# Optimization experiments

Measured on AMD Instinct MI355X. Metric: run time of the kernel, lower is better.

The kernel has to match this reference:

```python
import jax, jax.numpy as jnp
import numpy as np

EMBD_SIZE = 128
NUM_HEADS = 8
HEAD_SIZE = 16

def setup_inputs() -> dict:
    key = jax.random.key(0)
    ks = jax.random.split(key, 6)
    B, S = 8, 2048
    x = jax.random.normal(ks[0], (B, S, EMBD_SIZE), dtype=jnp.float32)
    # per-head Linear weights, torch layout [out, in] stacked over heads -> [H, hs, E]
    sc = 1.0 / np.sqrt(EMBD_SIZE)
    Wk = jax.random.normal(ks[1], (NUM_HEADS, HEAD_SIZE, EMBD_SIZE), dtype=jnp.float32) * sc
    Wq = jax.random.normal(ks[2], (NUM_HEADS, HEAD_SIZE, EMBD_SIZE), dtype=jnp.float32) * sc
    Wv = jax.random.normal(ks[3], (NUM_HEADS, HEAD_SIZE, EMBD_SIZE), dtype=jnp.float32) * sc
    Wp = jax.random.normal(ks[4], (EMBD_SIZE, NUM_HEADS * HEAD_SIZE), dtype=jnp.float32) * sc
    bp = jax.random.normal(ks[5], (EMBD_SIZE,), dtype=jnp.float32) * 0.01
    return {"x": x, "Wk": Wk, "Wq": Wq, "Wv": Wv, "Wp": Wp, "bp": bp}

def reference(x, Wk, Wq, Wv, Wp, bp):
    # x: [B,S,E]; W{k,q,v}: [H,hs,E]; Wp: [E,H*hs]
    B, S, E = x.shape
    H, hs, _ = Wk.shape
    q = jnp.einsum('bse,hde->bhsd', x, Wq)
    k = jnp.einsum('bse,hde->bhsd', x, Wk)
    v = jnp.einsum('bse,hde->bhsd', x, Wv)
    # NOTE: original code MULTIPLIES by sqrt(head_size) (k.shape[-1]**0.5)
    scores = jnp.einsum('bhsd,bhtd->bhst', q, k) * (hs ** 0.5)
    wei = jax.nn.softmax(scores, axis=-1)  # dropout is identity in eval mode
    out = jnp.einsum('bhst,bhtd->bhsd', wei, v)
    # concat heads along last dim: [B,S,H*hs]
    out = out.transpose(0, 2, 1, 3).reshape(B, S, H * hs)
    return out @ Wp.T + bp
```

## Files before the change

### kernel.cpp

```cpp
#include <hip/hip_runtime.h>
#include <hip/hip_bf16.h>

constexpr int Bb  = 8;
constexpr int Ss  = 2048;
constexpr int Ee  = 128;
constexpr int Hh  = 8;
constexpr int HSs = 16;
constexpr int QKVSZ = Bb * Hh * Ss * HSs;

typedef _Float16 f16;
typedef __attribute__((ext_vector_type(8)))  _Float16 f16x8;
typedef __attribute__((ext_vector_type(16))) float f32x16;

constexpr float QSCALE = 5.770780163555854f;

__device__ __forceinline__ unsigned pack_rtz(float lo, float hi) {
    union { __fp16 __attribute__((ext_vector_type(2))) h; unsigned u; } c;
    c.h = __builtin_amdgcn_cvt_pkrtz(lo, hi);
    return c.u;
}
__device__ __forceinline__ unsigned pack_rne(float lo, float hi) {
    union { __attribute__((ext_vector_type(2))) _Float16 h; unsigned u; } c;
    c.h[0] = (f16)lo; c.h[1] = (f16)hi;
    return c.u;
}

__global__ __launch_bounds__(256) void prep_w(
    const float* __restrict__ Wq, const float* __restrict__ Wk,
    const float* __restrict__ Wv, const float* __restrict__ Wp,
    f16* __restrict__ wh)
{
    int i = (blockIdx.x * 256 + threadIdx.x) * 4;
    const float* src = (i < 16384) ? (Wq + i)
                     : (i < 32768) ? (Wk + i - 16384)
                     : (i < 49152) ? (Wv + i - 32768) : (Wp + i - 49152);
    float4 v = *(const float4*)src;
    union { f16 h[4]; uint2 u; } c;
    c.h[0] = (f16)v.x; c.h[1] = (f16)v.y; c.h[2] = (f16)v.z; c.h[3] = (f16)v.w;
    *(uint2*)(wh + i) = c.u;
}

__global__ __launch_bounds__(256) void qkv_kernel(
    const float* __restrict__ x, const f16* __restrict__ wh,
    f16* __restrict__ qo, f16* __restrict__ ko, f16* __restrict__ vo)
{
    constexpr int LDW = 136;
    __shared__ __align__(16) f16 Xs[32 * LDW];

    const int mat = blockIdx.y;
    const int rowbase = blockIdx.x * 32;

    for (int idx = threadIdx.x; idx < 32 * 32; idx += 256) {
        const int r = idx >> 5, cp = idx & 31;
        float4 v = *(const float4*)(x + (size_t)(rowbase + r) * Ee + cp * 4);
        union { f16 h[4]; uint2 u; } c;
        c.h[0] = (f16)v.x; c.h[1] = (f16)v.y; c.h[2] = (f16)v.z; c.h[3] = (f16)v.w;
        *(uint2*)&Xs[r * LDW + cp * 4] = c.u;
    }
    __syncthreads();

    const int wv_ = threadIdx.x >> 6, lane = threadIdx.x & 63;
    const int h = lane >> 5, n31 = lane & 31;

    f16x8 A[8];
#pragma unroll
    for (int t = 0; t < 8; ++t)
        A[t] = *(const f16x8*)&Xs[n31 * LDW + 16 * t + 8 * h];

    const int c = wv_ * 32 + n31;
    const f16* wr = wh + mat * 16384 + (size_t)c * Ee + 8 * h;
    f32x16 acc = {};
#pragma unroll
    for (int t = 0; t < 8; ++t)
        acc = __builtin_amdgcn_mfma_f32_32x32x16_f16(A[t], *(const f16x8*)(wr + 16 * t), acc, 0, 0, 0);

    const int b = rowbase >> 11;
    const int s0 = rowbase & 2047;
    const int head = c >> 4, d = c & 15;
    const int bh = b * Hh + head;

    if (mat < 2) {
        f16* dst = (mat == 0) ? qo : ko;
        const float scale = (mat == 1) ? QSCALE : 1.f;
#pragma unroll
        for (int r = 0; r < 16; ++r) {
            const int s = s0 + (r & 3) + 8 * (r >> 2) + 4 * h;
            dst[((size_t)bh * Ss + s) * HSs + d] = (f16)(acc[r] * scale);
        }
    } else {
        const int it = s0 >> 6, g0 = (s0 >> 4) & 3;
        f16* vb = vo + (size_t)bh * 65536 + it * 2048;
#pragma unroll
        for (int rq = 0; rq < 4; ++rq) {
            union { f16 hv[4]; uint2 u; } pk4;
#pragma unroll
            for (int i = 0; i < 4; ++i) pk4.hv[i] = (f16)acc[4 * rq + i];
            *(uint2*)(vb + (g0 + (rq >> 1)) * 512 + (d + 32 * (rq & 1)) * 8 + 4 * h) = pk4.u;
        }
        for (int i = threadIdx.x; i < 512; i += 256) {
            const int gp = i >> 8, hd = (i >> 5) & 7, cc = i & 31;
            const int lanep = (cc < 16) ? 16 + cc : 32 + cc;
            const unsigned one2 = 0x3C003C00u;
            uint4 val = ((cc & 15) == 0) ? (uint4){one2, one2, one2, one2}
                                         : (uint4){0, 0, 0, 0};
            *(uint4*)(vo + (size_t)(b * Hh + hd) * 65536 + it * 2048
                      + (g0 + gp) * 512 + lanep * 8) = val;
        }
    }
}

__device__ __forceinline__ void cb_exchange(const unsigned* pw, int h,
                                            f16x8& Blo, f16x8& Bhi) {
    unsigned exa = (unsigned)__shfl_xor((int)(h ? pw[0] : pw[2]), 32, 64);
    unsigned exb = (unsigned)__shfl_xor((int)(h ? pw[1] : pw[3]), 32, 64);
    unsigned exc = (unsigned)__shfl_xor((int)(h ? pw[4] : pw[6]), 32, 64);
    unsigned exd = (unsigned)__shfl_xor((int)(h ? pw[5] : pw[7]), 32, 64);
    union { unsigned u[4]; f16x8 v; } B1, B2;
    if (h == 0) {
        B1.u[0] = pw[0]; B1.u[1] = pw[1]; B1.u[2] = exa; B1.u[3] = exb;
        B2.u[0] = pw[4]; B2.u[1] = pw[5]; B2.u[2] = exc; B2.u[3] = exd;
    } else {
        B1.u[0] = exa; B1.u[1] = exb; B1.u[2] = pw[2]; B1.u[3] = pw[3];
        B2.u[0] = exc; B2.u[1] = exd; B2.u[2] = pw[6]; B2.u[3] = pw[7];
    }
    Blo = B1.v; Bhi = B2.v;
}

__global__ __launch_bounds__(64, 4) void attn_kernel(
    const f16* __restrict__ qg, const f16* __restrict__ kg,
    const f16* __restrict__ vg, f16* __restrict__ og)
{
    const int blk  = blockIdx.x;
    const int bh   = (blk & 7) * 8 + (blk >> 9);
    const int qblk = (blk >> 3) & 63;
    const int lane = threadIdx.x;
    const int h    = lane >> 5;
    const int q31  = lane & 31;
    const int qbase = qblk * 32;

    const f16x8 qf = *(const f16x8*)(qg + ((size_t)bh * Ss + qbase + q31) * HSs + 8 * h);

    const f16* pk = kg + (size_t)bh * Ss * HSs + q31 * 16 + 8 * h;
    const f16* pv = vg + (size_t)bh * 65536 + lane * 8;

    f16x8 ka0 = *(const f16x8*)pk;
    f16x8 ka1 = *(const f16x8*)(pk + 512);
    f16x8 va0 = *(const f16x8*)(pv);
    f16x8 va1 = *(const f16x8*)(pv + 512);
    f16x8 va2 = *(const f16x8*)(pv + 1024);
    f16x8 va3 = *(const f16x8*)(pv + 1536);

    f32x16 acc = {};
    const f32x16 z16 = {};
    float m = -1e30f;

    for (int it = 0; it < Ss / 64; ++it) {
        f16x8 nk0, nk1, nv0, nv1, nv2, nv3;
        if (it < Ss / 64 - 1) {
            pk += 1024; pv += 2048;
            nk0 = *(const f16x8*)pk;
            nk1 = *(const f16x8*)(pk + 512);
            nv0 = *(const f16x8*)(pv);
            nv1 = *(const f16x8*)(pv + 512);
            nv2 = *(const f16x8*)(pv + 1024);
            nv3 = *(const f16x8*)(pv + 1536);
        }

        f32x16 st0 = __builtin_amdgcn_mfma_f32_32x32x16_f16(ka0, qf, z16, 0, 0, 0);
        f32x16 st1 = __builtin_amdgcn_mfma_f32_32x32x16_f16(ka1, qf, z16, 0, 0, 0);

        float mx = st0[0];
#pragma unroll
        for (int t = 1; t < 16; ++t) mx = fmaxf(mx, st0[t]);
#pragma unroll
        for (int t = 0; t < 16; ++t) mx = fmaxf(mx, st1[t]);
        mx = fmaxf(mx, __shfl_xor(mx, 32, 64));
        const float mnew = fmaxf(m, mx);
        const float corr = __builtin_amdgcn_exp2f(m - mnew);
#pragma unroll
        for (int r = 0; r < 9; ++r) acc[r] *= corr;
        m = mnew;

#pragma unroll
        for (int t = 0; t < 16; ++t) st0[t] = __builtin_amdgcn_exp2f(st0[t] - mnew);
#pragma unroll
        for (int t = 0; t < 16; ++t) st1[t] = __builtin_amdgcn_exp2f(st1[t] - mnew);
        unsigned pw0[8], pw1[8];
#pragma unroll
        for (int r = 0; r < 8; ++r) pw0[r] = pack_rtz(st0[2 * r], st0[2 * r + 1]);
#pragma unroll
        for (int r = 0; r < 8; ++r) pw1[r] = pack_rtz(st1[2 * r], st1[2 * r + 1]);
        f16x8 B1, B2, B3, B4;
        cb_exchange(pw0, h, B1, B2);
        cb_exchange(pw1, h, B3, B4);

        acc = __builtin_amdgcn_mfma_f32_32x32x16_f16(va0, B1, acc, 0, 0, 0);
        acc = __builtin_amdgcn_mfma_f32_32x32x16_f16(va1, B2, acc, 0, 0, 0);
        acc = __builtin_amdgcn_mfma_f32_32x32x16_f16(va2, B3, acc, 0, 0, 0);
        acc = __builtin_amdgcn_mfma_f32_32x32x16_f16(va3, B4, acc, 0, 0, 0);

        ka0 = nk0; ka1 = nk1;
        va0 = nv0; va1 = nv1; va2 = nv2; va3 = nv3;
    }

    const float l = acc[8] + __shfl_xor(acc[8], 32, 64);
    const float inv = 1.f / l;
    const int b = bh >> 3, head = bh & 7;
    f16* op = og + ((size_t)b * Ss + qbase + q31) * Ee + head * HSs;
    uint2 lo = { pack_rne(acc[0] * inv, acc[1] * inv), pack_rne(acc[2] * inv, acc[3] * inv) };
    uint2 hi = { pack_rne(acc[4] * inv, acc[5] * inv), pack_rne(acc[6] * inv, acc[7] * inv) };
    *(uint2*)(op + 4 * h)     = lo;
    *(uint2*)(op + 8 + 4 * h) = hi;
}

__global__ __launch_bounds__(256) void proj_kernel(
    const f16* __restrict__ oh, const f16* __restrict__ wph,
    const float* __restrict__ bp, float* __restrict__ out)
{
    constexpr int LDW = 136;
    __shared__ __align__(16) f16 Os[32 * LDW];
    const int rowbase = blockIdx.x * 32;

    for (int idx = threadIdx.x; idx < 512; idx += 256) {
        const int r = idx >> 4, cp = idx & 15;
        *(f16x8*)&Os[r * LDW + cp * 8] =
            *(const f16x8*)(oh + (size_t)(rowbase + r) * Ee + cp * 8);
    }
    __syncthreads();

    const int wv_ = threadIdx.x >> 6, lane = threadIdx.x & 63;
    const int h = lane >> 5, n31 = lane & 31;

    f16x8 A[8];
#pragma unroll
    for (int t = 0; t < 8; ++t)
        A[t] = *(const f16x8*)&Os[n31 * LDW + 16 * t + 8 * h];

    const int e = wv_ * 32 + n31;
    const f16* wr = wph + (size_t)e * Ee + 8 * h;
    f32x16 acc = {};
#pragma unroll
    for (int t = 0; t < 8; ++t)
        acc = __builtin_amdgcn_mfma_f32_32x32x16_f16(A[t], *(const f16x8*)(wr + 16 * t), acc, 0, 0, 0);

    const float bias = bp[e];
#pragma unroll
    for (int r = 0; r < 16; ++r) {
        const int R = rowbase + (r & 3) + 8 * (r >> 2) + 4 * h;
        out[(size_t)R * Ee + e] = acc[r] + bias;
    }
}

extern "C" void kernel_launch(void* const* d_in, const int* in_sizes, int n_in,
                              void* d_out, int out_size, void* d_ws, size_t ws_size,
                              hipStream_t stream)
{
    const float* x  = (const float*)d_in[0];
    const float* Wk = (const float*)d_in[1];
    const float* Wq = (const float*)d_in[2];
    const float* Wv = (const float*)d_in[3];
    const float* Wp = (const float*)d_in[4];
    const float* bp = (const float*)d_in[5];
    float* out = (float*)d_out;

    f16* ws = (f16*)d_ws;
    f16* qh = ws;
    f16* kh = ws + (size_t)QKVSZ;
    f16* vh = ws + (size_t)2 * QKVSZ;
    f16* oh = ws + (size_t)4 * QKVSZ;
    f16* wh = ws + (size_t)5 * QKVSZ;

    prep_w<<<64, 256, 0, stream>>>(Wq, Wk, Wv, Wp, wh);
    qkv_kernel<<<dim3(Bb * Ss / 32, 3), 256, 0, stream>>>(x, wh, qh, kh, vh);
    attn_kernel<<<Bb * Hh * (Ss / 32), 64, 0, stream>>>(qh, kh, vh, oh);
    proj_kernel<<<Bb * Ss / 32, 256, 0, stream>>>(oh, wh + 49152, bp, out);
}
```

Before: 137.6 us.

## Split attention KV range across two waves and fuse QKV into one pass

The attention kernel now runs two waves per block, each covering half the key/value sequence. Their partial softmax states are merged through shared memory, which doubles parallelism per query tile and halves the serial loop length. The QKV kernel computes all three projections in one block, reusing the loaded x tile instead of reloading it for each matrix. V is staged through shared memory so it can be written as coalesced 16-byte stores, and the constant ones/zeros padding of the V layout moves into the prep kernel. The cost is an extra shared-memory combine step and more register pressure in the attention blocks.

Result: slower. 321.0 us (+133.2%).

```diff
diff --git a/kernel.cpp b/kernel.cpp
--- a/kernel.cpp
+++ b/kernel.cpp
@@ -25,19 +25,30 @@
     return c.u;
 }
 
-__global__ __launch_bounds__(256) void prep_w(
+__global__ __launch_bounds__(256) void prep_kernel(
     const float* __restrict__ Wq, const float* __restrict__ Wk,
     const float* __restrict__ Wv, const float* __restrict__ Wp,
-    f16* __restrict__ wh)
-{
-    int i = (blockIdx.x * 256 + threadIdx.x) * 4;
-    const float* src = (i < 16384) ? (Wq + i)
-                     : (i < 32768) ? (Wk + i - 16384)
-                     : (i < 49152) ? (Wv + i - 32768) : (Wp + i - 49152);
-    float4 v = *(const float4*)src;
-    union { f16 h[4]; uint2 u; } c;
-    c.h[0] = (f16)v.x; c.h[1] = (f16)v.y; c.h[2] = (f16)v.z; c.h[3] = (f16)v.w;
-    *(uint2*)(wh + i) = c.u;
+    f16* __restrict__ wh, f16* __restrict__ vo)
+{
+    const int idx = blockIdx.x * 256 + threadIdx.x;
+    if (idx < 16384) {
+        const int i = idx * 4;
+        const float* src = (i < 16384) ? (Wq + i)
+                         : (i < 32768) ? (Wk + i - 16384)
+                         : (i < 49152) ? (Wv + i - 32768) : (Wp + i - 49152);
+        float4 v = *(const float4*)src;
+        union { f16 h[4]; uint2 u; } c;
+        c.h[0] = (f16)v.x; c.h[1] = (f16)v.y; c.h[2] = (f16)v.z; c.h[3] = (f16)v.w;
+        *(uint2*)(wh + i) = c.u;
+    } else {
+        const int p = idx - 16384;
+        const int lane32 = p & 31, g = (p >> 5) & 3, it = (p >> 7) & 31, bh = p >> 12;
+        const int lanep = 16 + (lane32 & 15) + (lane32 >> 4) * 32;
+        const unsigned one2 = 0x3C003C00u;
+        uint4 val = ((lane32 & 15) == 0) ? (uint4){one2, one2, one2, one2}
+                                         : (uint4){0, 0, 0, 0};
+        *(uint4*)(vo + (size_t)bh * 65536 + it * 2048 + g * 512 + lanep * 8) = val;
+    }
 }
 
 __global__ __launch_bounds__(256) void qkv_kernel(
@@ -47,7 +58,6 @@
     constexpr int LDW = 136;
     __shared__ __align__(16) f16 Xs[32 * LDW];
 
-    const int mat = blockIdx.y;
     const int rowbase = blockIdx.x * 32;
 
     for (int idx = threadIdx.x; idx < 32 * 32; idx += 256) {
@@ -66,20 +76,34 @@
 #pragma unroll
     for (int t = 0; t < 8; ++t)
         A[t] = *(const f16x8*)&Xs[n31 * LDW + 16 * t + 8 * h];
+    __syncthreads();
 
     const int c = wv_ * 32 + n31;
-    const f16* wr = wh + mat * 16384 + (size_t)c * Ee + 8 * h;
-    f32x16 acc = {};
-#pragma unroll
-    for (int t = 0; t < 8; ++t)
-        acc = __builtin_amdgcn_mfma_f32_32x32x16_f16(A[t], *(const f16x8*)(wr + 16 * t), acc, 0, 0, 0);
-
     const int b = rowbase >> 11;
     const int s0 = rowbase & 2047;
     const int head = c >> 4, d = c & 15;
     const int bh = b * Hh + head;
 
-    if (mat < 2) {
+    {
+        const f16* wr = wh + 2 * 16384 + (size_t)c * Ee + 8 * h;
+        f32x16 acc = {};
+#pragma unroll
+        for (int t = 0; t < 8; ++t)
+            acc = __builtin_amdgcn_mfma_f32_32x32x16_f16(A[t], *(const f16x8*)(wr + 16 * t), acc, 0, 0, 0);
+#pragma unroll
+        for (int r = 0; r < 16; ++r) {
+            const int row = (r & 3) + 8 * (r >> 2) + 4 * h;
+            Xs[row * LDW + c] = (f16)acc[r];
+        }
+    }
+
+#pragma unroll
+    for (int mat = 0; mat < 2; ++mat) {
+        const f16* wr = wh + mat * 16384 + (size_t)c * Ee + 8 * h;
+        f32x16 acc = {};
+#pragma unroll
+        for (int t = 0; t < 8; ++t)
+            acc = __builtin_amdgcn_mfma_f32_32x32x16_f16(A[t], *(const f16x8*)(wr + 16 * t), acc, 0, 0, 0);
         f16* dst = (mat == 0) ? qo : ko;
         const float scale = (mat == 1) ? QSCALE : 1.f;
 #pragma unroll
@@ -87,25 +111,18 @@
             const int s = s0 + (r & 3) + 8 * (r >> 2) + 4 * h;
             dst[((size_t)bh * Ss + s) * HSs + d] = (f16)(acc[r] * scale);
         }
-    } else {
-        const int it = s0 >> 6, g0 = (s0 >> 4) & 3;
-        f16* vb = vo + (size_t)bh * 65536 + it * 2048;
-#pragma unroll
-        for (int rq = 0; rq < 4; ++rq) {
-            union { f16 hv[4]; uint2 u; } pk4;
-#pragma unroll
-            for (int i = 0; i < 4; ++i) pk4.hv[i] = (f16)acc[4 * rq + i];
-            *(uint2*)(vb + (g0 + (rq >> 1)) * 512 + (d + 32 * (rq & 1)) * 8 + 4 * h) = pk4.u;
-        }
-        for (int i = threadIdx.x; i < 512; i += 256) {
-            const int gp = i >> 8, hd = (i >> 5) & 7, cc = i & 31;
-            const int lanep = (cc < 16) ? 16 + cc : 32 + cc;
-            const unsigned one2 = 0x3C003C00u;
-            uint4 val = ((cc & 15) == 0) ? (uint4){one2, one2, one2, one2}
-                                         : (uint4){0, 0, 0, 0};
-            *(uint4*)(vo + (size_t)(b * Hh + hd) * 65536 + it * 2048
-                      + (g0 + gp) * 512 + lanep * 8) = val;
-        }
+    }
+    __syncthreads();
+
+    const int it = s0 >> 6, g0 = (s0 >> 4) & 3;
+    for (int p = threadIdx.x; p < 512; p += 256) {
+        const int gl = p >> 8, hd = (p >> 5) & 7, dd = (p >> 1) & 15, eh = p & 1;
+        union { f16 hv[8]; uint4 u; } pkt;
+#pragma unroll
+        for (int j = 0; j < 8; ++j)
+            pkt.hv[j] = Xs[(gl * 16 + eh * 8 + j) * LDW + hd * 16 + dd];
+        *(uint4*)(vo + (size_t)(b * Hh + hd) * 65536 + it * 2048
+                  + (g0 + gl) * 512 + (dd + 32 * eh) * 8) = pkt.u;
     }
 }
 
@@ -126,22 +143,25 @@
     Blo = B1.v; Bhi = B2.v;
 }
 
-__global__ __launch_bounds__(64, 4) void attn_kernel(
+__global__ __launch_bounds__(128, 6) void attn_kernel(
     const f16* __restrict__ qg, const f16* __restrict__ kg,
     const f16* __restrict__ vg, f16* __restrict__ og)
 {
+    __shared__ float cmb[32 * 20];
+
     const int blk  = blockIdx.x;
     const int bh   = (blk & 7) * 8 + (blk >> 9);
     const int qblk = (blk >> 3) & 63;
-    const int lane = threadIdx.x;
+    const int wv_  = threadIdx.x >> 6;
+    const int lane = threadIdx.x & 63;
     const int h    = lane >> 5;
     const int q31  = lane & 31;
     const int qbase = qblk * 32;
 
     const f16x8 qf = *(const f16x8*)(qg + ((size_t)bh * Ss + qbase + q31) * HSs + 8 * h);
 
-    const f16* pk = kg + (size_t)bh * Ss * HSs + q31 * 16 + 8 * h;
-    const f16* pv = vg + (size_t)bh * 65536 + lane * 8;
+    const f16* pk = kg + (size_t)bh * Ss * HSs + wv_ * 1024 * HSs + q31 * 16 + 8 * h;
+    const f16* pv = vg + (size_t)bh * 65536 + wv_ * 32768 + lane * 8;
 
     f16x8 ka0 = *(const f16x8*)pk;
     f16x8 ka1 = *(const f16x8*)(pk + 512);
@@ -154,9 +174,9 @@
     const f32x16 z16 = {};
     float m = -1e30f;
 
-    for (int it = 0; it < Ss / 64; ++it) {
+    for (int it = 0; it < 16; ++it) {
         f16x8 nk0, nk1, nv0, nv1, nv2, nv3;
-        if (it < Ss / 64 - 1) {
+        if (it < 15) {
             pk += 1024; pv += 2048;
             nk0 = *(const f16x8*)pk;
             nk1 = *(const f16x8*)(pk + 512);
@@ -169,11 +189,13 @@
         f32x16 st0 = __builtin_amdgcn_mfma_f32_32x32x16_f16(ka0, qf, z16, 0, 0, 0);
         f32x16 st1 = __builtin_amdgcn_mfma_f32_32x32x16_f16(ka1, qf, z16, 0, 0, 0);
 
-        float mx = st0[0];
-#pragma unroll
-        for (int t = 1; t < 16; ++t) mx = fmaxf(mx, st0[t]);
-#pragma unroll
-        for (int t = 0; t < 16; ++t) mx = fmaxf(mx, st1[t]);
+        float t0[8];
+#pragma unroll
+        for (int t = 0; t < 8; ++t)
+            t0[t] = fmaxf(fmaxf(st0[t], st0[t + 8]), fmaxf(st1[t], st1[t + 8]));
+#pragma unroll
+        for (int t = 0; t < 4; ++t) t0[t] = fmaxf(t0[t], t0[t + 4]);
+        float mx = fmaxf(fmaxf(t0[0], t0[1]), fmaxf(t0[2], t0[3]));
         mx = fmaxf(mx, __shfl_xor(mx, 32, 64));
         const float mnew = fmaxf(m, mx);
         const float corr = __builtin_amdgcn_exp2f(m - mnew);
@@ -203,14 +225,36 @@
         va0 = nv0; va1 = nv1; va2 = nv2; va3 = nv3;
     }
 
-    const float l = acc[8] + __shfl_xor(acc[8], 32, 64);
-    const float inv = 1.f / l;
-    const int b = bh >> 3, head = bh & 7;
-    f16* op = og + ((size_t)b * Ss + qbase + q31) * Ee + head * HSs;
-    uint2 lo = { pack_rne(acc[0] * inv, acc[1] * inv), pack_rne(acc[2] * inv, acc[3] * inv) };
-    uint2 hi = { pack_rne(acc[4] * inv, acc[5] * inv), pack_rne(acc[6] * inv, acc[7] * inv) };
-    *(uint2*)(op + 4 * h)     = lo;
-    *(uint2*)(op + 8 + 4 * h) = hi;
+    const float lp = acc[8] + __shfl_xor(acc[8], 32, 64);
+
+    if (wv_ == 1) {
+        float* base = &cmb[q31 * 20];
+#pragma unroll
+        for (int j = 0; j < 4; ++j) { base[4 * h + j] = acc[j]; base[8 + 4 * h + j] = acc[4 + j]; }
+        base[16] = lp; base[17] = m;
+    }
+    __syncthreads();
+    if (wv_ == 0) {
+        const float* base = &cmb[q31 * 20];
+        const float l2 = base[16], m2 = base[17];
+        const float M  = fmaxf(m, m2);
+        const float c1 = __builtin_amdgcn_exp2f(m - M);
+        const float c2 = __builtin_amdgcn_exp2f(m2 - M);
+        const float l  = lp * c1 + l2 * c2;
+        const float inv = 1.f / l;
+        float o[8];
+#pragma unroll
+        for (int j = 0; j < 4; ++j) {
+            o[j]     = (acc[j]     * c1 + base[4 * h + j]     * c2) * inv;
+            o[4 + j] = (acc[4 + j] * c1 + base[8 + 4 * h + j] * c2) * inv;
+        }
+        const int b = bh >> 3, head = bh & 7;
+        f16* op = og + ((size_t)b * Ss + qbase + q31) * Ee + head * HSs;
+        uint2 lo = { pack_rne(o[0], o[1]), pack_rne(o[2], o[3]) };
+        uint2 hi = { pack_rne(o[4], o[5]), pack_rne(o[6], o[7]) };
+        *(uint2*)(op + 4 * h)     = lo;
+        *(uint2*)(op + 8 + 4 * h) = hi;
+    }
 }
 
 __global__ __launch_bounds__(256) void proj_kernel(
@@ -270,8 +314,8 @@
     f16* oh = ws + (size_t)4 * QKVSZ;
     f16* wh = ws + (size_t)5 * QKVSZ;
 
-    prep_w<<<64, 256, 0, stream>>>(Wq, Wk, Wv, Wp, wh);
-    qkv_kernel<<<dim3(Bb * Ss / 32, 3), 256, 0, stream>>>(x, wh, qh, kh, vh);
-    attn_kernel<<<Bb * Hh * (Ss / 32), 64, 0, stream>>>(qh, kh, vh, oh);
+    prep_kernel<<<1088, 256, 0, stream>>>(Wq, Wk, Wv, Wp, wh, vh);
+    qkv_kernel<<<Bb * Ss / 32, 256, 0, stream>>>(x, wh, qh, kh, vh);
+    attn_kernel<<<Bb * Hh * (Ss / 32), 128, 0, stream>>>(qh, kh, vh, oh);
     proj_kernel<<<Bb * Ss / 32, 256, 0, stream>>>(oh, wh + 49152, bp, out);
 }
```
